# Performance work log

Hardware: AMD Instinct MI355X
Metric: run time of the kernel (lower is better)

Reference implementation:

```python
import jax, jax.numpy as jnp
import numpy as np

N, E = 100000, 1600000
D_IN, D_HID, D_OUT, P_HID = 256, 128, 128, 512
BN_EPS = 1e-5


def setup_inputs():
    key = jax.random.key(0)
    ks = jax.random.split(key, 16)
    rn = lambda k, sh, s: jax.random.normal(k, sh, jnp.float32) * s
    inp = {
        "x1": rn(ks[0], (N, D_IN), 1.0),
        "x2": rn(ks[1], (N, D_IN), 1.0),
        "edge_index_v1": jax.random.randint(ks[2], (2, E), 0, N, dtype=jnp.int32),
        "edge_index_v2": jax.random.randint(ks[3], (2, E), 0, N, dtype=jnp.int32),
    }
    # student (s_) and teacher (t_) encoder params: GCN weight/bias, BN gamma/beta, PReLU a
    for i, p in enumerate(("s", "t")):
        kk = jax.random.split(ks[4 + i], 4)
        inp[p + "_W1"] = rn(kk[0], (D_IN, D_HID), (2.0 / (D_IN + D_HID)) ** 0.5)
        inp[p + "_b1"] = jnp.zeros((D_HID,), jnp.float32)
        inp[p + "_g1"] = jnp.ones((D_HID,), jnp.float32)
        inp[p + "_be1"] = jnp.zeros((D_HID,), jnp.float32)
        inp[p + "_a1"] = jnp.float32(0.25)
        inp[p + "_W2"] = rn(kk[1], (D_HID, D_OUT), (2.0 / (D_HID + D_OUT)) ** 0.5)
        inp[p + "_b2"] = jnp.zeros((D_OUT,), jnp.float32)
        inp[p + "_g2"] = jnp.ones((D_OUT,), jnp.float32)
        inp[p + "_be2"] = jnp.zeros((D_OUT,), jnp.float32)
        inp[p + "_a2"] = jnp.float32(0.25)
    kk = jax.random.split(ks[6], 2)
    inp["p_W1"] = rn(kk[0], (D_OUT, P_HID), (2.0 / (D_OUT + P_HID)) ** 0.5)
    inp["p_b1"] = jnp.full((P_HID,), 0.01, jnp.float32)
    inp["p_a"] = jnp.float32(0.25)
    inp["p_W2"] = rn(kk[1], (P_HID, D_OUT), (2.0 / (P_HID + D_OUT)) ** 0.5)
    inp["p_b2"] = jnp.full((D_OUT,), 0.01, jnp.float32)
    return inp


def _add_self_loops(edge_index, n):
    loops = jnp.arange(n, dtype=edge_index.dtype)
    return (jnp.concatenate([edge_index[0], loops]),
            jnp.concatenate([edge_index[1], loops]))


def _gcn(x, src, dst, W, b):
    # torch_geometric GCNConv: symmetric deg^-1/2 norm, transform then scatter-add, bias after
    n = x.shape[0]
    ew = jnp.ones(src.shape, x.dtype)
    deg = jax.ops.segment_sum(ew, dst, num_segments=n)
    dinv = jnp.where(deg > 0, jax.lax.rsqrt(deg), 0.0)
    norm = (dinv[src] * dinv[dst])[:, None]  # [E+N, 1]
    h = x @ W  # [N, d_out]
    out = jax.ops.segment_sum(h[src] * norm, dst, num_segments=n)
    return out + b


def _bn(x, g, b):
    mu = x.mean(0)
    var = ((x - mu) ** 2).mean(0)  # biased var, training-mode batch stats
    return (x - mu) * jax.lax.rsqrt(var + BN_EPS) * g + b


def _prelu(x, a):
    return jnp.where(x >= 0, x, a * x)


def _encoder(x, src, dst, p):
    W1, b1, g1, be1, a1, W2, b2, g2, be2, a2 = p
    h = _prelu(_bn(_gcn(x, src, dst, W1, b1), g1, be1), a1)
    return _prelu(_bn(_gcn(h, src, dst, W2, b2), g2, be2), a2)


def _normalize(x):
    return x / jnp.maximum(jnp.linalg.norm(x, axis=-1, keepdims=True), 1e-12)


def reference(x1, x2, edge_index_v1, edge_index_v2,
              s_W1, s_b1, s_g1, s_be1, s_a1, s_W2, s_b2, s_g2, s_be2, s_a2,
              t_W1, t_b1, t_g1, t_be1, t_a1, t_W2, t_b2, t_g2, t_be2, t_a2,
              p_W1, p_b1, p_a, p_W2, p_b2):
    n = x1.shape[0]
    src1, dst1 = _add_self_loops(edge_index_v1, n)
    src2, dst2 = _add_self_loops(edge_index_v2, n)
    sp = (s_W1, s_b1, s_g1, s_be1, s_a1, s_W2, s_b2, s_g2, s_be2, s_a2)
    tp = (t_W1, t_b1, t_g1, t_be1, t_a1, t_W2, t_b2, t_g2, t_be2, t_a2)

    v1_student = _encoder(x1, src1, dst1, sp)
    v2_student = _encoder(x2, src2, dst2, sp)

    def _pred(h):
        return _prelu(h @ p_W1 + p_b1, p_a) @ p_W2 + p_b2

    v1_pred = _pred(v1_student)
    v2_pred = _pred(v2_student)

    v1_teacher = jax.lax.stop_gradient(_encoder(x1, src1, dst1, tp))
    v2_teacher = jax.lax.stop_gradient(_encoder(x2, src2, dst2, tp))

    loss1 = 2.0 - 2.0 * (_normalize(v1_pred) * _normalize(v2_teacher)).sum(-1)
    loss2 = 2.0 - 2.0 * (_normalize(v2_pred) * _normalize(v1_teacher)).sum(-1)
    return (v1_student, v2_student, (loss1 + loss2).mean())
```

## Files before the change

kernel.cpp:

```cpp
#include <hip/hip_runtime.h>

#define NN 100000
#define EE 1600000
#define ENN (EE + NN)
#define DIN 256
#define DH 128
#define PH 512

static constexpr float BN_EPS_C = 1e-5f;

typedef __bf16 bf16_t;
typedef bf16_t bf16x8 __attribute__((ext_vector_type(8)));
typedef bf16_t bf16x4 __attribute__((ext_vector_type(4)));
typedef float floatx4 __attribute__((ext_vector_type(4)));


__global__ void init_deg_k(int* __restrict__ deg1, int* __restrict__ deg2) {
    int i = blockIdx.x * 256 + threadIdx.x;
    if (i < NN) { deg1[i] = 1; deg2[i] = 1; }
}

__global__ void count_deg_k(const int* __restrict__ dst, int* __restrict__ deg) {
    int e = blockIdx.x * 256 + threadIdx.x;
    if (e < EE) atomicAdd(&deg[dst[e]], 1);
}

__global__ void dinv_k(const int* __restrict__ deg, float* __restrict__ dinv) {
    int i = blockIdx.x * 256 + threadIdx.x;
    if (i < NN) dinv[i] = rsqrtf((float)deg[i]);
}

__global__ void scan1_k(const int* __restrict__ deg, int* __restrict__ bsum) {
    __shared__ int sh[256];
    int t = threadIdx.x;
    int base = blockIdx.x * 1024 + t * 4;
    int s = 0;
#pragma unroll
    for (int i = 0; i < 4; i++) { int idx = base + i; if (idx < NN) s += deg[idx]; }
    sh[t] = s; __syncthreads();
    for (int off = 128; off > 0; off >>= 1) { if (t < off) sh[t] += sh[t + off]; __syncthreads(); }
    if (t == 0) bsum[blockIdx.x] = sh[0];
}

__global__ void scan2_k(int* __restrict__ bsum, int nb) {
    __shared__ int sh[128];
    int t = threadIdx.x;
    int my = (t < nb) ? bsum[t] : 0;
    sh[t] = my; __syncthreads();
    for (int off = 1; off < 128; off <<= 1) {
        int v = (t >= off) ? sh[t - off] : 0;
        __syncthreads(); sh[t] += v; __syncthreads();
    }
    if (t < nb) bsum[t] = sh[t] - my;
}

__global__ void scan3_k(const int* __restrict__ deg, const int* __restrict__ bsum,
                        int* __restrict__ rowoff) {
    __shared__ int sh[256];
    int t = threadIdx.x;
    int base = blockIdx.x * 1024 + t * 4;
    int v[4]; int s = 0;
#pragma unroll
    for (int i = 0; i < 4; i++) { int idx = base + i; v[i] = (idx < NN) ? deg[idx] : 0; s += v[i]; }
    int my = s;
    sh[t] = s; __syncthreads();
    for (int off = 1; off < 256; off <<= 1) {
        int x = (t >= off) ? sh[t - off] : 0;
        __syncthreads(); sh[t] += x; __syncthreads();
    }
    int run = sh[t] - my + bsum[blockIdx.x];
#pragma unroll
    for (int i = 0; i < 4; i++) { int idx = base + i; if (idx < NN) rowoff[idx] = run; run += v[i]; }
    if (blockIdx.x == 0 && t == 0) rowoff[NN] = ENN;
}

__global__ void csr_init_k(const int* __restrict__ rowoff, const float* __restrict__ dinv,
                           int* __restrict__ cursor, int2* __restrict__ csre) {
    int i = blockIdx.x * 256 + threadIdx.x;
    if (i < NN) {
        int p = rowoff[i];
        float d = dinv[i];
        csre[p] = make_int2(i, __float_as_int(d * d));
        cursor[i] = p + 1;
    }
}

__global__ void csr_place_k(const int* __restrict__ src, const int* __restrict__ dst,
                            const float* __restrict__ dinv, int* __restrict__ cursor,
                            int2* __restrict__ csre) {
    int e = blockIdx.x * 256 + threadIdx.x;
    if (e < EE) {
        int s = src[e], d = dst[e];
        int p = atomicAdd(&cursor[d], 1);
        csre[p] = make_int2(s, __float_as_int(dinv[s] * dinv[d]));
    }
}


__global__ __launch_bounds__(256) void gather256_k(
    const int* __restrict__ ro, const int2* __restrict__ csre,
    const bf16_t* __restrict__ h,
    const float* __restrict__ bs, const float* __restrict__ bt,
    float* __restrict__ out)
{
    int wv = threadIdx.x >> 6, lane = threadIdx.x & 63;
    int d = blockIdx.x * 4 + wv;
    if (d >= NN) return;
    int beg = ro[d], end = ro[d + 1];
    int c4 = lane * 4;
    float a0 = 0.f, a1 = 0.f, a2 = 0.f, a3 = 0.f;
    for (int e = beg; e < end; ++e) {
        int2 ew = csre[e];
        float w = __int_as_float(ew.y);
        uint2 pr = *(const uint2*)(h + (size_t)ew.x * 256 + c4);
        a0 += w * __uint_as_float(pr.x << 16);
        a1 += w * __uint_as_float(pr.x & 0xffff0000u);
        a2 += w * __uint_as_float(pr.y << 16);
        a3 += w * __uint_as_float(pr.y & 0xffff0000u);
    }
    float b0 = (c4 < 128) ? bs[c4]     : bt[c4 - 128];
    float b1 = (c4 < 128) ? bs[c4 + 1] : bt[c4 - 127];
    float b2 = (c4 < 128) ? bs[c4 + 2] : bt[c4 - 126];
    float b3 = (c4 < 128) ? bs[c4 + 3] : bt[c4 - 125];
    float4 r = make_float4(a0 + b0, a1 + b1, a2 + b2, a3 + b3);
    *(float4*)&out[(size_t)d * 256 + c4] = r;
}


#define GSTAT 1024
#define SROWS ((NN + GSTAT - 1) / GSTAT)

__global__ __launch_bounds__(256) void bn_stats_cat_k(const float* __restrict__ x,
                                                      float* __restrict__ stats) {
    __shared__ float sh[2][4][256];
    int t = threadIdx.x;
    int wv = t >> 6, lane = t & 63;
    int c4 = lane * 4;
    int rend = (blockIdx.x + 1) * SROWS; if (rend > NN) rend = NN;
    float4 s = make_float4(0.f, 0.f, 0.f, 0.f);
    float4 q = make_float4(0.f, 0.f, 0.f, 0.f);
    for (int r = blockIdx.x * SROWS + wv; r < rend; r += 4) {
        float4 v = *(const float4*)&x[(size_t)r * 256 + c4];
        s.x += v.x; s.y += v.y; s.z += v.z; s.w += v.w;
        q.x += v.x * v.x; q.y += v.y * v.y; q.z += v.z * v.z; q.w += v.w * v.w;
    }
    *(float4*)&sh[0][wv][c4] = s;
    *(float4*)&sh[1][wv][c4] = q;
    __syncthreads();
    if (t < 128) {
        int which = t >> 6;
        int c = (t & 63) * 4;
        float4 a  = *(float4*)&sh[which][0][c];
        float4 b  = *(float4*)&sh[which][1][c];
        float4 cc = *(float4*)&sh[which][2][c];
        float4 d  = *(float4*)&sh[which][3][c];
        atomicAdd(&stats[which * 256 + c],     a.x + b.x + cc.x + d.x);
        atomicAdd(&stats[which * 256 + c + 1], a.y + b.y + cc.y + d.y);
        atomicAdd(&stats[which * 256 + c + 2], a.z + b.z + cc.z + d.z);
        atomicAdd(&stats[which * 256 + c + 3], a.w + b.w + cc.w + d.w);
    }
}

__global__ void bn_prelu_cat_k(const float* __restrict__ x, const float* __restrict__ stats,
                               const float* __restrict__ gs, const float* __restrict__ gt,
                               const float* __restrict__ bes, const float* __restrict__ bet,
                               const float* __restrict__ as_, const float* __restrict__ at_,
                               bf16_t* __restrict__ out) {
    size_t i4 = ((size_t)blockIdx.x * 256 + threadIdx.x) * 4;
    if (i4 < (size_t)NN * 256) {
        int c = (int)(i4 & 255);
        bool st = c < 128;
        int cb = st ? c : c - 128;
        const float* gp  = st ? gs  : gt;
        const float* bep = st ? bes : bet;
        float al = st ? as_[0] : at_[0];
        float4 v = *(const float4*)&x[i4];
        float vv[4] = {v.x, v.y, v.z, v.w};
        bf16x4 o;
#pragma unroll
        for (int j = 0; j < 4; j++) {
            float mu  = stats[c + j] * (1.0f / NN);
            float var = stats[256 + c + j] * (1.0f / NN) - mu * mu;
            float sc  = rsqrtf(var + BN_EPS_C) * gp[cb + j];
            float r   = (vv[j] - mu) * sc + bep[cb + j];
            r = r >= 0.f ? r : al * r;
            o[j] = (bf16_t)r;
        }
        *(bf16x4*)&out[i4] = o;
    }
}

__global__ void bn_prelu_out_k(const float* __restrict__ x, const float* __restrict__ stats,
                               const float* __restrict__ gs, const float* __restrict__ gt,
                               const float* __restrict__ bes, const float* __restrict__ bet,
                               const float* __restrict__ as_, const float* __restrict__ at_,
                               float* __restrict__ outs, bf16_t* __restrict__ outsb,
                               bf16_t* __restrict__ outt) {
    size_t i4 = ((size_t)blockIdx.x * 256 + threadIdx.x) * 4;
    if (i4 >= (size_t)NN * 256) return;
    int c = (int)(i4 & 255);
    size_t r = i4 >> 8;
    bool st = c < 128;
    int cb = st ? c : c - 128;
    const float* gp  = st ? gs  : gt;
    const float* bep = st ? bes : bet;
    float al = st ? as_[0] : at_[0];
    float4 v = *(const float4*)&x[i4];
    float vv[4] = {v.x, v.y, v.z, v.w};
    float res[4];
    bf16x4 o;
#pragma unroll
    for (int j = 0; j < 4; j++) {
        float mu  = stats[c + j] * (1.0f / NN);
        float var = stats[256 + c + j] * (1.0f / NN) - mu * mu;
        float sc  = rsqrtf(var + BN_EPS_C) * gp[cb + j];
        float rr  = (vv[j] - mu) * sc + bep[cb + j];
        rr = rr >= 0.f ? rr : al * rr;
        res[j] = rr;
        o[j] = (bf16_t)rr;
    }
    if (st) {
        *(float4*)&outs[r * 128 + cb] = make_float4(res[0], res[1], res[2], res[3]);
        *(bf16x4*)&outsb[r * 128 + cb] = o;
    } else {
        *(bf16x4*)&outt[r * 128 + cb] = o;
    }
}


__global__ void wt_k(const float* __restrict__ W, bf16_t* __restrict__ Wt, int K, int M) {
    int i = blockIdx.x * 256 + threadIdx.x;
    if (i < K * M) {
        int k = i / M, m = i - k * M;
        Wt[(size_t)m * K + k] = (bf16_t)W[i];
    }
}


#define LDT 40

template <int K, typename AT, typename OT, bool BIAS, bool PRELU>
__global__ __launch_bounds__(256) void mgemm_k(
    const AT* __restrict__ A, int lda, const bf16_t* __restrict__ Wt,
    OT* __restrict__ C, int ldc, int nrows,
    const float* __restrict__ bias, const float* __restrict__ prelu_a)
{
    __shared__ __align__(16) bf16_t sA[128 * LDT];
    __shared__ __align__(16) bf16_t sB[128 * LDT];
    const int tid = threadIdx.x;
    const int row0 = blockIdx.x * 128;
    const int col0 = blockIdx.y * 128;
    const int lane = tid & 63, quad = lane >> 4, l15 = lane & 15;
    const int wv = tid >> 6, wrow = wv >> 1, wcol = wv & 1;

    const int sr = tid >> 1;
    const int sh = (tid & 1) * 16;

    floatx4 acc[4][4] = {};

    const int arow = row0 + sr;
    const bool arow_ok = arow < nrows;
    const AT*     ag = A  + (size_t)arow * lda + sh;
    const bf16_t* bg = Wt + (size_t)(col0 + sr) * K + sh;

    for (int k0 = 0; k0 < K; k0 += 32) {
        __syncthreads();
        if constexpr (sizeof(AT) == 4) {
            float4 f0, f1, f2, f3;
            if (arow_ok) {
                const float4* p4 = (const float4*)(ag + k0);
                f0 = p4[0]; f1 = p4[1]; f2 = p4[2]; f3 = p4[3];
            } else {
                f0 = f1 = f2 = f3 = make_float4(0.f, 0.f, 0.f, 0.f);
            }
            bf16x8 u0 = {(bf16_t)f0.x, (bf16_t)f0.y, (bf16_t)f0.z, (bf16_t)f0.w,
                         (bf16_t)f1.x, (bf16_t)f1.y, (bf16_t)f1.z, (bf16_t)f1.w};
            bf16x8 u1 = {(bf16_t)f2.x, (bf16_t)f2.y, (bf16_t)f2.z, (bf16_t)f2.w,
                         (bf16_t)f3.x, (bf16_t)f3.y, (bf16_t)f3.z, (bf16_t)f3.w};
            *(bf16x8*)&sA[sr * LDT + sh]     = u0;
            *(bf16x8*)&sA[sr * LDT + sh + 8] = u1;
        } else {
            int4 w0, w1;
            if (arow_ok) {
                const int4* p4 = (const int4*)(ag + k0);
                w0 = p4[0]; w1 = p4[1];
            } else {
                w0 = make_int4(0, 0, 0, 0); w1 = make_int4(0, 0, 0, 0);
            }
            *(int4*)&sA[sr * LDT + sh]     = w0;
            *(int4*)&sA[sr * LDT + sh + 8] = w1;
        }
        {
            const int4* wp = (const int4*)(bg + k0);
            int4 w0 = wp[0], w1 = wp[1];
            *(int4*)&sB[sr * LDT + sh]     = w0;
            *(int4*)&sB[sr * LDT + sh + 8] = w1;
        }
        __syncthreads();

        bf16x8 af[4], bf[4];
#pragma unroll
        for (int r = 0; r < 4; r++)
            af[r] = *(const bf16x8*)&sA[(wrow * 64 + r * 16 + l15) * LDT + quad * 8];
#pragma unroll
        for (int c = 0; c < 4; c++)
            bf[c] = *(const bf16x8*)&sB[(wcol * 64 + c * 16 + l15) * LDT + quad * 8];
#pragma unroll
        for (int r = 0; r < 4; r++)
#pragma unroll
            for (int c = 0; c < 4; c++)
                acc[r][c] = __builtin_amdgcn_mfma_f32_16x16x32_bf16(af[r], bf[c], acc[r][c], 0, 0, 0);
    }

    const float alpha = PRELU ? prelu_a[0] : 0.f;
#pragma unroll
    for (int r = 0; r < 4; r++) {
        const int rbase = wrow * 64 + r * 16 + quad * 4;
#pragma unroll
        for (int c = 0; c < 4; c++) {
            const int gcol = col0 + wcol * 64 + c * 16 + l15;
            const float bv = BIAS ? bias[gcol] : 0.f;
#pragma unroll
            for (int j = 0; j < 4; j++) {
                const int grow = row0 + rbase + j;
                if (grow < nrows) {
                    float v = acc[r][c][j] + bv;
                    if (PRELU) v = v >= 0.f ? v : alpha * v;
                    C[(size_t)grow * ldc + gcol] = (OT)v;
                }
            }
        }
    }
}


__global__ void loss_partial_k(const bf16_t* __restrict__ v1p, const bf16_t* __restrict__ v2t,
                               const bf16_t* __restrict__ v2p, const bf16_t* __restrict__ v1t,
                               float* __restrict__ partials) {
    __shared__ float shw[4];
    int t = threadIdx.x;
    int lane = t & 63, wv = t >> 6;
    float wsum = 0.f;
    for (int it = 0; it < 8; ++it) {
        int r = blockIdx.x * 32 + wv * 8 + it;
        if (r < NN) {
            const bf16_t* A = v1p + (size_t)r * DH;
            const bf16_t* B = v2t + (size_t)r * DH;
            const bf16_t* Cc = v2p + (size_t)r * DH;
            const bf16_t* D = v1t + (size_t)r * DH;
            float a0 = (float)A[lane], a1 = (float)A[lane + 64];
            float b0 = (float)B[lane], b1 = (float)B[lane + 64];
            float c0 = (float)Cc[lane], c1 = (float)Cc[lane + 64];
            float d0 = (float)D[lane], d1 = (float)D[lane + 64];
            float dot1 = a0 * b0 + a1 * b1;
            float na = a0 * a0 + a1 * a1, nb = b0 * b0 + b1 * b1;
            float dot2 = c0 * d0 + c1 * d1;
            float nc = c0 * c0 + c1 * c1, nd = d0 * d0 + d1 * d1;
            for (int off = 32; off > 0; off >>= 1) {
                dot1 += __shfl_down(dot1, off);
                na   += __shfl_down(na, off);
                nb   += __shfl_down(nb, off);
                dot2 += __shfl_down(dot2, off);
                nc   += __shfl_down(nc, off);
                nd   += __shfl_down(nd, off);
            }
            if (lane == 0) {
                float den1 = fmaxf(sqrtf(na), 1e-12f) * fmaxf(sqrtf(nb), 1e-12f);
                float den2 = fmaxf(sqrtf(nc), 1e-12f) * fmaxf(sqrtf(nd), 1e-12f);
                wsum += 4.f - 2.f * dot1 / den1 - 2.f * dot2 / den2;
            }
        }
    }
    if (lane == 0) shw[wv] = wsum;
    __syncthreads();
    if (t == 0) partials[blockIdx.x] = shw[0] + shw[1] + shw[2] + shw[3];
}

__global__ void loss_final_k(const float* __restrict__ partials, int n, float* __restrict__ out) {
    __shared__ float sh[256];
    int t = threadIdx.x;
    float s = 0.f;
    for (int i = t; i < n; i += 256) s += partials[i];
    sh[t] = s; __syncthreads();
    for (int off = 128; off > 0; off >>= 1) { if (t < off) sh[t] += sh[t + off]; __syncthreads(); }
    if (t == 0) out[0] = sh[0] / (float)NN;
}


extern "C" void kernel_launch(void* const* d_in, const int* in_sizes, int n_in,
                              void* d_out, int out_size, void* d_ws, size_t ws_size,
                              hipStream_t stream) {
    const float* x1 = (const float*)d_in[0];
    const float* x2 = (const float*)d_in[1];
    const int* ei1 = (const int*)d_in[2];
    const int* ei2 = (const int*)d_in[3];
    const float* sp[10]; for (int i = 0; i < 10; i++) sp[i] = (const float*)d_in[4 + i];
    const float* tp[10]; for (int i = 0; i < 10; i++) tp[i] = (const float*)d_in[14 + i];
    const float* pW1 = (const float*)d_in[24];
    const float* pb1 = (const float*)d_in[25];
    const float* pa  = (const float*)d_in[26];
    const float* pW2 = (const float*)d_in[27];
    const float* pb2 = (const float*)d_in[28];

    float* out = (float*)d_out;
    float* v1s = out;
    float* v2s = out + (size_t)NN * DH;
    float* lossp = out + (size_t)2 * NN * DH;

    char* p = (char*)d_ws;
    auto alloc = [&](size_t bytes) { char* r = p; p += (bytes + 255) & ~(size_t)255; return r; };
    int*   deg1   = (int*)alloc(NN * 4);
    int*   deg2   = (int*)alloc(NN * 4);
    float* dinv1  = (float*)alloc(NN * 4);
    float* dinv2  = (float*)alloc(NN * 4);
    int*   ro1    = (int*)alloc((NN + 1) * 4);
    int*   ro2    = (int*)alloc((NN + 1) * 4);
    int*   cursor = (int*)alloc(NN * 4);
    int*   bsum   = (int*)alloc(128 * 4);
    int2*  csre1  = (int2*)alloc((size_t)ENN * 8);
    int2*  csre2  = (int2*)alloc((size_t)ENN * 8);
    bf16_t* hcat  = (bf16_t*)alloc((size_t)NN * 256 * 2);
    bf16_t* h2    = (bf16_t*)alloc((size_t)NN * 256 * 2);
    float*  agg   = (float*)alloc((size_t)NN * 256 * 4);
    bf16_t* v1sb  = (bf16_t*)alloc((size_t)NN * DH * 2);
    bf16_t* v2sb  = (bf16_t*)alloc((size_t)NN * DH * 2);
    bf16_t* v1t   = (bf16_t*)alloc((size_t)NN * DH * 2);
    bf16_t* v2t   = (bf16_t*)alloc((size_t)NN * DH * 2);
    bf16_t* v1p   = (bf16_t*)alloc((size_t)NN * DH * 2);
    bf16_t* v2p   = (bf16_t*)alloc((size_t)NN * DH * 2);
    float* stats  = (float*)alloc(4 * 512 * 4);
    float* partials = (float*)alloc(4096 * 4);
    bf16_t* W1cat = (bf16_t*)alloc((size_t)2 * DIN * DH * 2);
    bf16_t* sW2t = (bf16_t*)alloc((size_t)DH * DH * 2);
    bf16_t* tW2t = (bf16_t*)alloc((size_t)DH * DH * 2);
    bf16_t* pW1t = (bf16_t*)alloc((size_t)DH * PH * 2);
    bf16_t* pW2t = (bf16_t*)alloc((size_t)PH * DH * 2);

    const int GN256 = (NN + 255) / 256;
    const int GE256 = (EE + 255) / 256;
    const int NB_SCAN = (NN + 1023) / 1024;
    const int GMM = (NN + 127) / 128;
    const int GG = (NN + 3) / 4;
    const int GEL4 = (NN * 256 / 4 + 255) / 256;

    hipMemsetAsync(stats, 0, 4 * 512 * 4, stream);

    wt_k<<<(DIN * DH + 255) / 256, 256, 0, stream>>>(sp[0], W1cat, DIN, DH);
    wt_k<<<(DIN * DH + 255) / 256, 256, 0, stream>>>(tp[0], W1cat + (size_t)DH * DIN, DIN, DH);
    wt_k<<<(DH * DH + 255) / 256, 256, 0, stream>>>(sp[5], sW2t, DH, DH);
    wt_k<<<(DH * DH + 255) / 256, 256, 0, stream>>>(tp[5], tW2t, DH, DH);
    wt_k<<<(DH * PH + 255) / 256, 256, 0, stream>>>(pW1, pW1t, DH, PH);
    wt_k<<<(PH * DH + 255) / 256, 256, 0, stream>>>(pW2, pW2t, PH, DH);

    init_deg_k<<<GN256, 256, 0, stream>>>(deg1, deg2);
    count_deg_k<<<GE256, 256, 0, stream>>>(ei1 + EE, deg1);
    count_deg_k<<<GE256, 256, 0, stream>>>(ei2 + EE, deg2);
    dinv_k<<<GN256, 256, 0, stream>>>(deg1, dinv1);
    dinv_k<<<GN256, 256, 0, stream>>>(deg2, dinv2);

    scan1_k<<<NB_SCAN, 256, 0, stream>>>(deg1, bsum);
    scan2_k<<<1, 128, 0, stream>>>(bsum, NB_SCAN);
    scan3_k<<<NB_SCAN, 256, 0, stream>>>(deg1, bsum, ro1);
    csr_init_k<<<GN256, 256, 0, stream>>>(ro1, dinv1, cursor, csre1);
    csr_place_k<<<GE256, 256, 0, stream>>>(ei1, ei1 + EE, dinv1, cursor, csre1);

    scan1_k<<<NB_SCAN, 256, 0, stream>>>(deg2, bsum);
    scan2_k<<<1, 128, 0, stream>>>(bsum, NB_SCAN);
    scan3_k<<<NB_SCAN, 256, 0, stream>>>(deg2, bsum, ro2);
    csr_init_k<<<GN256, 256, 0, stream>>>(ro2, dinv2, cursor, csre2);
    csr_place_k<<<GE256, 256, 0, stream>>>(ei2, ei2 + EE, dinv2, cursor, csre2);

    auto encoder = [&](const float* x, const int* ro, const int2* csre,
                       float* vs_out, bf16_t* vsb, bf16_t* vt, int set) {
        mgemm_k<DIN, float, bf16_t, false, false><<<dim3(GMM, 2), 256, 0, stream>>>(
            x, DIN, W1cat, hcat, 256, NN, nullptr, nullptr);
        gather256_k<<<GG, 256, 0, stream>>>(ro, csre, hcat, sp[1], tp[1], agg);
        bn_stats_cat_k<<<GSTAT, 256, 0, stream>>>(agg, stats + set * 512);
        bn_prelu_cat_k<<<GEL4, 256, 0, stream>>>(agg, stats + set * 512,
            sp[2], tp[2], sp[3], tp[3], sp[4], tp[4], hcat);
        mgemm_k<DH, bf16_t, bf16_t, false, false><<<dim3(GMM, 1), 256, 0, stream>>>(
            hcat, 256, sW2t, h2, 256, NN, nullptr, nullptr);
        mgemm_k<DH, bf16_t, bf16_t, false, false><<<dim3(GMM, 1), 256, 0, stream>>>(
            hcat + 128, 256, tW2t, h2 + 128, 256, NN, nullptr, nullptr);
        gather256_k<<<GG, 256, 0, stream>>>(ro, csre, h2, sp[6], tp[6], agg);
        bn_stats_cat_k<<<GSTAT, 256, 0, stream>>>(agg, stats + (set + 1) * 512);
        bn_prelu_out_k<<<GEL4, 256, 0, stream>>>(agg, stats + (set + 1) * 512,
            sp[7], tp[7], sp[8], tp[8], sp[9], tp[9], vs_out, vsb, vt);
    };

    encoder(x1, ro1, csre1, v1s, v1sb, v1t, 0);
    encoder(x2, ro2, csre2, v2s, v2sb, v2t, 2);

    bf16_t* hid = (bf16_t*)agg;
    auto predictor = [&](const bf16_t* vin, bf16_t* vout) {
        mgemm_k<DH, bf16_t, bf16_t, true, true><<<dim3(GMM, PH / 128), 256, 0, stream>>>(
            vin, DH, pW1t, hid, PH, NN, pb1, pa);
        mgemm_k<PH, bf16_t, bf16_t, true, false><<<dim3(GMM, 1), 256, 0, stream>>>(
            hid, PH, pW2t, vout, DH, NN, pb2, nullptr);
    };
    predictor(v1sb, v1p);
    predictor(v2sb, v2p);

    const int GL = (NN + 31) / 32;
    loss_partial_k<<<GL, 256, 0, stream>>>(v1p, v2t, v2p, v1t, partials);
    loss_final_k<<<1, 256, 0, stream>>>(partials, GL, lossp);
}
```

Measured before the change: 2.301 ms.

## Split gather wavefront into half-waves with 16-byte loads and merge layer-2 GEMMs

The gather kernel now has each half-wave cover a full 256-column row using 8-element 16-byte loads. Each iteration issues four edges' worth of independent loads per half, and the halves are combined with a cross-half shuffle. This raises memory-level parallelism and load width for the irregular row gathers, at the cost of more registers and wasted clamped loads on low-degree nodes. The two layer-2 student and teacher GEMMs are also merged into one launch using a concatenated weight and a per-blockIdx.y A-column offset.

```diff
diff --git a/kernel.cpp b/kernel.cpp
--- a/kernel.cpp
+++ b/kernel.cpp
@@ -107,23 +107,59 @@
     int d = blockIdx.x * 4 + wv;
     if (d >= NN) return;
     int beg = ro[d], end = ro[d + 1];
-    int c4 = lane * 4;
-    float a0 = 0.f, a1 = 0.f, a2 = 0.f, a3 = 0.f;
-    for (int e = beg; e < end; ++e) {
-        int2 ew = csre[e];
-        float w = __int_as_float(ew.y);
-        uint2 pr = *(const uint2*)(h + (size_t)ew.x * 256 + c4);
-        a0 += w * __uint_as_float(pr.x << 16);
-        a1 += w * __uint_as_float(pr.x & 0xffff0000u);
-        a2 += w * __uint_as_float(pr.y << 16);
-        a3 += w * __uint_as_float(pr.y & 0xffff0000u);
-    }
-    float b0 = (c4 < 128) ? bs[c4]     : bt[c4 - 128];
-    float b1 = (c4 < 128) ? bs[c4 + 1] : bt[c4 - 127];
-    float b2 = (c4 < 128) ? bs[c4 + 2] : bt[c4 - 126];
-    float b3 = (c4 < 128) ? bs[c4 + 3] : bt[c4 - 125];
-    float4 r = make_float4(a0 + b0, a1 + b1, a2 + b2, a3 + b3);
-    *(float4*)&out[(size_t)d * 256 + c4] = r;
+    int half = lane >> 5;
+    int l32 = lane & 31;
+    int c8 = l32 * 8;
+    const bf16_t* hp = h + c8;
+    float acc[8] = {0.f, 0.f, 0.f, 0.f, 0.f, 0.f, 0.f, 0.f};
+
+    for (int e = beg; e < end; e += 8) {
+        int i0 = e + half;
+        int i1 = i0 + 2, i2 = i0 + 4, i3 = i0 + 6;
+        bool val0 = i0 < end, val1 = i1 < end, val2 = i2 < end, val3 = i3 < end;
+        int j0 = val0 ? i0 : end - 1;
+        int j1 = val1 ? i1 : end - 1;
+        int j2 = val2 ? i2 : end - 1;
+        int j3 = val3 ? i3 : end - 1;
+        int2 w0 = csre[j0];
+        int2 w1 = csre[j1];
+        int2 w2 = csre[j2];
+        int2 w3 = csre[j3];
+        uint4 p0 = *(const uint4*)(hp + w0.x * 256);
+        uint4 p1 = *(const uint4*)(hp + w1.x * 256);
+        uint4 p2 = *(const uint4*)(hp + w2.x * 256);
+        uint4 p3 = *(const uint4*)(hp + w3.x * 256);
+        float f0 = val0 ? __int_as_float(w0.y) : 0.f;
+        float f1 = val1 ? __int_as_float(w1.y) : 0.f;
+        float f2 = val2 ? __int_as_float(w2.y) : 0.f;
+        float f3 = val3 ? __int_as_float(w3.y) : 0.f;
+#define GACC(P, F) \
+        acc[0] += (F) * __uint_as_float((P).x << 16); \
+        acc[1] += (F) * __uint_as_float((P).x & 0xffff0000u); \
+        acc[2] += (F) * __uint_as_float((P).y << 16); \
+        acc[3] += (F) * __uint_as_float((P).y & 0xffff0000u); \
+        acc[4] += (F) * __uint_as_float((P).z << 16); \
+        acc[5] += (F) * __uint_as_float((P).z & 0xffff0000u); \
+        acc[6] += (F) * __uint_as_float((P).w << 16); \
+        acc[7] += (F) * __uint_as_float((P).w & 0xffff0000u);
+        GACC(p0, f0)
+        GACC(p1, f1)
+        GACC(p2, f2)
+        GACC(p3, f3)
+#undef GACC
+    }
+
+#pragma unroll
+    for (int j = 0; j < 8; j++) acc[j] += __shfl_xor(acc[j], 32);
+
+    int cB = c8 + half * 4;
+    int o = half * 4;
+    float b0 = (cB < 128) ? bs[cB]     : bt[cB - 128];
+    float b1 = (cB < 128) ? bs[cB + 1] : bt[cB - 127];
+    float b2 = (cB < 128) ? bs[cB + 2] : bt[cB - 126];
+    float b3 = (cB < 128) ? bs[cB + 3] : bt[cB - 125];
+    float4 r = make_float4(acc[o] + b0, acc[o + 1] + b1, acc[o + 2] + b2, acc[o + 3] + b3);
+    *(float4*)&out[(size_t)d * 256 + cB] = r;
 }
 
 
@@ -242,7 +278,7 @@
 template <int K, typename AT, typename OT, bool BIAS, bool PRELU>
 __global__ __launch_bounds__(256) void mgemm_k(
     const AT* __restrict__ A, int lda, const bf16_t* __restrict__ Wt,
-    OT* __restrict__ C, int ldc, int nrows,
+    OT* __restrict__ C, int ldc, int nrows, int aoffy,
     const float* __restrict__ bias, const float* __restrict__ prelu_a)
 {
     __shared__ __align__(16) bf16_t sA[128 * LDT];
@@ -260,7 +296,7 @@
 
     const int arow = row0 + sr;
     const bool arow_ok = arow < nrows;
-    const AT*     ag = A  + (size_t)arow * lda + sh;
+    const AT*     ag = A  + (size_t)arow * lda + sh + blockIdx.y * aoffy;
     const bf16_t* bg = Wt + (size_t)(col0 + sr) * K + sh;
 
     for (int k0 = 0; k0 < K; k0 += 32) {
@@ -431,8 +467,7 @@
     float* stats  = (float*)alloc(4 * 512 * 4);
     float* partials = (float*)alloc(4096 * 4);
     bf16_t* W1cat = (bf16_t*)alloc((size_t)2 * DIN * DH * 2);
-    bf16_t* sW2t = (bf16_t*)alloc((size_t)DH * DH * 2);
-    bf16_t* tW2t = (bf16_t*)alloc((size_t)DH * DH * 2);
+    bf16_t* W2cat = (bf16_t*)alloc((size_t)2 * DH * DH * 2);
     bf16_t* pW1t = (bf16_t*)alloc((size_t)DH * PH * 2);
     bf16_t* pW2t = (bf16_t*)alloc((size_t)PH * DH * 2);
 
@@ -447,8 +482,8 @@
 
     wt_k<<<(DIN * DH + 255) / 256, 256, 0, stream>>>(sp[0], W1cat, DIN, DH);
     wt_k<<<(DIN * DH + 255) / 256, 256, 0, stream>>>(tp[0], W1cat + (size_t)DH * DIN, DIN, DH);
-    wt_k<<<(DH * DH + 255) / 256, 256, 0, stream>>>(sp[5], sW2t, DH, DH);
-    wt_k<<<(DH * DH + 255) / 256, 256, 0, stream>>>(tp[5], tW2t, DH, DH);
+    wt_k<<<(DH * DH + 255) / 256, 256, 0, stream>>>(sp[5], W2cat, DH, DH);
+    wt_k<<<(DH * DH + 255) / 256, 256, 0, stream>>>(tp[5], W2cat + (size_t)DH * DH, DH, DH);
     wt_k<<<(DH * PH + 255) / 256, 256, 0, stream>>>(pW1, pW1t, DH, PH);
     wt_k<<<(PH * DH + 255) / 256, 256, 0, stream>>>(pW2, pW2t, PH, DH);
 
@@ -473,15 +508,13 @@
     auto encoder = [&](const float* x, const int* ro, const int2* csre,
                        float* vs_out, bf16_t* vsb, bf16_t* vt, int set) {
         mgemm_k<DIN, float, bf16_t, false, false><<<dim3(GMM, 2), 256, 0, stream>>>(
-            x, DIN, W1cat, hcat, 256, NN, nullptr, nullptr);
+            x, DIN, W1cat, hcat, 256, NN, 0, nullptr, nullptr);
         gather256_k<<<GG, 256, 0, stream>>>(ro, csre, hcat, sp[1], tp[1], agg);
         bn_stats_cat_k<<<GSTAT, 256, 0, stream>>>(agg, stats + set * 512);
         bn_prelu_cat_k<<<GEL4, 256, 0, stream>>>(agg, stats + set * 512,
             sp[2], tp[2], sp[3], tp[3], sp[4], tp[4], hcat);
-        mgemm_k<DH, bf16_t, bf16_t, false, false><<<dim3(GMM, 1), 256, 0, stream>>>(
-            hcat, 256, sW2t, h2, 256, NN, nullptr, nullptr);
-        mgemm_k<DH, bf16_t, bf16_t, false, false><<<dim3(GMM, 1), 256, 0, stream>>>(
-            hcat + 128, 256, tW2t, h2 + 128, 256, NN, nullptr, nullptr);
+        mgemm_k<DH, bf16_t, bf16_t, false, false><<<dim3(GMM, 2), 256, 0, stream>>>(
+            hcat, 256, W2cat, h2, 256, NN, 128, nullptr, nullptr);
         gather256_k<<<GG, 256, 0, stream>>>(ro, csre, h2, sp[6], tp[6], agg);
         bn_stats_cat_k<<<GSTAT, 256, 0, stream>>>(agg, stats + (set + 1) * 512);
         bn_prelu_out_k<<<GEL4, 256, 0, stream>>>(agg, stats + (set + 1) * 512,
@@ -494,9 +527,9 @@
     bf16_t* hid = (bf16_t*)agg;
     auto predictor = [&](const bf16_t* vin, bf16_t* vout) {
         mgemm_k<DH, bf16_t, bf16_t, true, true><<<dim3(GMM, PH / 128), 256, 0, stream>>>(
-            vin, DH, pW1t, hid, PH, NN, pb1, pa);
+            vin, DH, pW1t, hid, PH, NN, 0, pb1, pa);
         mgemm_k<PH, bf16_t, bf16_t, true, false><<<dim3(GMM, 1), 256, 0, stream>>>(
-            hid, PH, pW2t, vout, DH, NN, pb2, nullptr);
+            hid, PH, pW2t, vout, DH, NN, 0, pb2, nullptr);
     };
     predictor(v1sb, v1p);
     predictor(v2sb, v2p);
```

After: 2.041 ms. 11.3% less time.
